# Optimization experiments

Hardware: AMD Instinct MI355X
Metric: run time of the kernel (lower is better)

The kernel has to match this reference:

```python
import jax, jax.numpy as jnp
import numpy as np

OBS, ACT, HID, MIX, TOPK = 64, 16, 256, 16, 4
EPS = 1e-5

def _ln(x, g, b):
    m = jnp.mean(x, axis=-1, keepdims=True)
    v = jnp.mean(jnp.square(x - m), axis=-1, keepdims=True)
    return (x - m) * jax.lax.rsqrt(v + EPS) * g + b

def setup_inputs() -> dict:
    key = jax.random.key(0)
    ks = jax.random.split(key, 12)
    B = 16384
    D = OBS + ACT            # 80
    F = HID * MIX            # 4096
    s = lambda fan_in: 1.0 / np.sqrt(fan_in)
    return {
        "x": jax.random.normal(ks[0], (B, OBS), jnp.float32),
        "a": jax.random.normal(ks[1], (B, ACT), jnp.float32),
        "W1": jax.random.uniform(ks[2], (F, D), jnp.float32, -s(D), s(D)),
        "b1": jnp.zeros((F,), jnp.float32),
        "W2": jax.random.uniform(ks[3], (F, F), jnp.float32, -s(F), s(F)),
        "b2": jnp.zeros((F,), jnp.float32),
        "W3": jax.random.uniform(ks[4], (1, HID), jnp.float32, -s(HID), s(HID)),
        "b3": jnp.zeros((1,), jnp.float32),
        "g1": jnp.ones((F,), jnp.float32),
        "be1": jnp.zeros((F,), jnp.float32),
        "g2": jnp.ones((F,), jnp.float32),
        "be2": jnp.zeros((F,), jnp.float32),
        "Wg": jax.random.uniform(ks[5], (MIX, D), jnp.float32, -s(D), s(D)),
        "bg": jnp.zeros((MIX,), jnp.float32),
    }

def reference(x, a, W1, b1, W2, b2, W3, b3, g1, be1, g2, be2, Wg, bg):
    B = x.shape[0]
    xa = jnp.concatenate([x, a], axis=1)                      # [B, D]
    gate_scores = jax.nn.softmax(xa @ Wg.T + bg, axis=-1)     # [B, MIX]
    topk_vals, topk_idx = jax.lax.top_k(gate_scores, TOPK)    # [B, K]
    # renormalize top-k weights, scatter into dense score tensor
    topk_vals = topk_vals / jnp.sum(topk_vals, axis=-1, keepdims=True)
    scores = jnp.zeros_like(gate_scores).at[
        jnp.arange(B)[:, None], topk_idx].set(topk_vals)      # [B, MIX]
    h = jax.nn.relu(_ln(xa @ W1.T + b1, g1, be1))             # [B, HID*MIX]
    h = jax.nn.relu(_ln(h @ W2.T + b2, g2, be2))              # [B, HID*MIX]
    h = h.reshape(B, HID, MIX)                                # row-major, same as torch
    h = jnp.mean(h * scores[:, None, :], axis=-1)             # [B, HID]
    return h @ W3.T + b3                                      # [B, 1]
```

## Files before the change

### kernel.cpp

```cpp
#include <hip/hip_runtime.h>
#include <stdint.h>

#define OBS 64
#define ACTD 16
#define DIN 80
#define MIX 16
#define FF 4096
#define NB 16384
#define CHUNK 4096
#define KP 96
#define LNEPS 1e-5f

typedef float f32x4 __attribute__((ext_vector_type(4)));
typedef short bf16x8 __attribute__((ext_vector_type(8)));

__device__ __forceinline__ unsigned short f2bf(float f) {
    union { float f; uint32_t u; } v; v.f = f;
    uint32_t u = v.u;
    u += 0x7fff + ((u >> 16) & 1);
    return (unsigned short)(u >> 16);
}
__device__ __forceinline__ float bf2f(unsigned short h) {
    union { uint32_t u; float f; } v; v.u = ((uint32_t)h) << 16;
    return v.f;
}

__global__ __launch_bounds__(256) void k_conv(const float* __restrict__ W,
                                              unsigned short* __restrict__ O, int n4) {
    int i = blockIdx.x * 256 + threadIdx.x;
    if (i >= n4) return;
    float4 v = ((const float4*)W)[i];
    ushort4 o;
    o.x = f2bf(v.x); o.y = f2bf(v.y); o.z = f2bf(v.z); o.w = f2bf(v.w);
    ((ushort4*)O)[i] = o;
}

__global__ __launch_bounds__(256) void k_prep_x(const float* __restrict__ x, const float* __restrict__ a,
                                                unsigned short* __restrict__ xab) {
    int row = blockIdx.x * 256 + threadIdx.x;
    const float4* xp = (const float4*)(x + (size_t)row * OBS);
    unsigned short* o = xab + (size_t)row * KP;
#pragma unroll
    for (int i = 0; i < 16; ++i) {
        float4 v = xp[i];
        ushort4 u; u.x = f2bf(v.x); u.y = f2bf(v.y); u.z = f2bf(v.z); u.w = f2bf(v.w);
        ((ushort4*)o)[i] = u;
    }
    const float4* ap = (const float4*)(a + (size_t)row * ACTD);
#pragma unroll
    for (int i = 0; i < 4; ++i) {
        float4 v = ap[i];
        ushort4 u; u.x = f2bf(v.x); u.y = f2bf(v.y); u.z = f2bf(v.z); u.w = f2bf(v.w);
        ((ushort4*)(o + OBS))[i] = u;
    }
    ushort4 t0; t0.x = 0x3F80; t0.y = 0; t0.z = 0; t0.w = 0;
    ushort4 z;  z.x = 0; z.y = 0; z.z = 0; z.w = 0;
    ((ushort4*)(o + 80))[0] = t0;
    ((ushort4*)(o + 84))[0] = z;
    ((ushort4*)(o + 88))[0] = z;
    ((ushort4*)(o + 92))[0] = z;
}

__global__ __launch_bounds__(256) void k_prep_w1(const float* __restrict__ W1, const float* __restrict__ b1,
                                                 unsigned short* __restrict__ W1b) {
    int f = blockIdx.x * 256 + threadIdx.x;
    const float4* wp = (const float4*)(W1 + (size_t)f * DIN);
    unsigned short* o = W1b + (size_t)f * KP;
#pragma unroll
    for (int i = 0; i < 20; ++i) {
        float4 v = wp[i];
        ushort4 u; u.x = f2bf(v.x); u.y = f2bf(v.y); u.z = f2bf(v.z); u.w = f2bf(v.w);
        ((ushort4*)o)[i] = u;
    }
    ushort4 t0; t0.x = f2bf(b1[f]); t0.y = 0; t0.z = 0; t0.w = 0;
    ushort4 z;  z.x = 0; z.y = 0; z.z = 0; z.w = 0;
    ((ushort4*)(o + 80))[0] = t0;
    ((ushort4*)(o + 84))[0] = z;
    ((ushort4*)(o + 88))[0] = z;
    ((ushort4*)(o + 92))[0] = z;
}

__global__ __launch_bounds__(256) void k_gate(const float* __restrict__ x, const float* __restrict__ a,
                                              const float* __restrict__ Wg, const float* __restrict__ bg,
                                              float* __restrict__ scores) {
    __shared__ float wgs[MIX * DIN];
    __shared__ float bgs[MIX];
    int t = threadIdx.x;
    for (int e = t; e < MIX * DIN; e += 256) wgs[e] = Wg[e];
    if (t < MIX) bgs[t] = bg[t];
    __syncthreads();
    int row = blockIdx.x * 256 + t;
    float xa[DIN];
    const float4* xp = (const float4*)(x + (size_t)row * OBS);
#pragma unroll
    for (int i = 0; i < OBS / 4; ++i) {
        float4 v = xp[i];
        xa[i*4] = v.x; xa[i*4+1] = v.y; xa[i*4+2] = v.z; xa[i*4+3] = v.w;
    }
    const float4* ap = (const float4*)(a + (size_t)row * ACTD);
#pragma unroll
    for (int i = 0; i < ACTD / 4; ++i) {
        float4 v = ap[i];
        xa[OBS+i*4] = v.x; xa[OBS+i*4+1] = v.y; xa[OBS+i*4+2] = v.z; xa[OBS+i*4+3] = v.w;
    }
    double p[MIX];
    double mx = -1e300;
#pragma unroll
    for (int m = 0; m < MIX; ++m) {
        double acc = (double)bgs[m];
#pragma unroll
        for (int k = 0; k < DIN; ++k) acc += (double)xa[k] * (double)wgs[m*DIN + k];
        p[m] = acc;
        if (acc > mx) mx = acc;
    }
#pragma unroll
    for (int m = 0; m < MIX; ++m) p[m] = exp(p[m] - mx);
    unsigned used = 0;
    double s4 = 0.0;
#pragma unroll
    for (int j = 0; j < 4; ++j) {
        int best = 0; double bv = -1.0;
#pragma unroll
        for (int m = 0; m < MIX; ++m)
            if (!((used >> m) & 1) && p[m] > bv) { bv = p[m]; best = m; }
        used |= 1u << best;
        s4 += bv;
    }
    float* so = scores + (size_t)row * MIX;
#pragma unroll
    for (int m = 0; m < MIX; ++m)
        so[m] = ((used >> m) & 1) ? (float)(p[m] / s4) : 0.f;
}

__global__ __launch_bounds__(256) void k_gemm1(const unsigned short* __restrict__ A,
                                               const unsigned short* __restrict__ B,
                                               unsigned short* __restrict__ C,
                                               float* __restrict__ pstats) {
    __shared__ alignas(16) unsigned short As[128 * 32];
    __shared__ alignas(16) unsigned short Bs[128 * 32];
    int t = threadIdx.x;
    int pm = blockIdx.x & 31;
    int pn = blockIdx.x >> 5;
    int lane = t & 63, wid = t >> 6, wm = wid >> 1, wn = wid & 1;

    const unsigned short* Ap = A + (size_t)pm * 128 * KP;
    const unsigned short* Bp = B + (size_t)pn * 128 * KP;

    f32x4 acc[4][4] = {};

    for (int k0 = 0; k0 < KP; k0 += 32) {
#pragma unroll
        for (int i = 0; i < 2; ++i) {
            int u = t + i * 256;
            int row = u >> 2, p = u & 3;
            int ls = p ^ ((row >> 1) & 3);
            __builtin_amdgcn_global_load_lds(
                (const __attribute__((address_space(1))) void*)(Ap + (size_t)row * KP + k0 + ls * 8),
                (__attribute__((address_space(3))) void*)(As + u * 8), 16, 0, 0);
            __builtin_amdgcn_global_load_lds(
                (const __attribute__((address_space(1))) void*)(Bp + (size_t)row * KP + k0 + ls * 8),
                (__attribute__((address_space(3))) void*)(Bs + u * 8), 16, 0, 0);
        }
        __syncthreads();
        bf16x8 af[4], bfr[4];
#pragma unroll
        for (int mf = 0; mf < 4; ++mf) {
            int r = wm * 64 + mf * 16 + (lane & 15);
            int p = (lane >> 4) ^ ((r >> 1) & 3);
            af[mf] = *(const bf16x8*)(As + r * 32 + p * 8);
        }
#pragma unroll
        for (int nf = 0; nf < 4; ++nf) {
            int r = wn * 64 + nf * 16 + (lane & 15);
            int p = (lane >> 4) ^ ((r >> 1) & 3);
            bfr[nf] = *(const bf16x8*)(Bs + r * 32 + p * 8);
        }
#pragma unroll
        for (int mf = 0; mf < 4; ++mf)
#pragma unroll
            for (int nf = 0; nf < 4; ++nf)
                acc[mf][nf] = __builtin_amdgcn_mfma_f32_16x16x32_bf16(af[mf], bfr[nf], acc[mf][nf], 0, 0, 0);
        __syncthreads();
    }

    int rowbase = pm * 128 + wm * 64 + (lane >> 4) * 4;
    int colbase = pn * 128 + wn * 64 + (lane & 15);
#pragma unroll
    for (int mf = 0; mf < 4; ++mf) {
#pragma unroll
        for (int rr = 0; rr < 4; ++rr) {
            float ss = 0.f, qq = 0.f;
#pragma unroll
            for (int nf = 0; nf < 4; ++nf) {
                float v = acc[mf][nf][rr];
                ss += v; qq += v * v;
                C[(size_t)(rowbase + mf * 16 + rr) * FF + colbase + nf * 16] = f2bf(v);
            }
#pragma unroll
            for (int mask = 1; mask <= 8; mask <<= 1) {
                ss += __shfl_xor(ss, mask);
                qq += __shfl_xor(qq, mask);
            }
            if ((lane & 15) == 0) {
                int row = rowbase + mf * 16 + rr;
                int j = pn * 2 + wn;
                pstats[((size_t)row * 64 + j) * 2 + 0] = ss;
                pstats[((size_t)row * 64 + j) * 2 + 1] = qq;
            }
        }
    }
}

__global__ __launch_bounds__(256) void k_ln1(unsigned short* __restrict__ h1,
                                             const float* __restrict__ pstats,
                                             const float* __restrict__ g1, const float* __restrict__ be1) {
    __shared__ float st[8][2];
    int t = threadIdx.x;
    int r0 = blockIdx.x * 8;
    if (t < 8) {
        float s = 0.f, q = 0.f;
        const float* pp = pstats + (size_t)(r0 + t) * 128;
#pragma unroll
        for (int j = 0; j < 64; ++j) { s += pp[j * 2]; q += pp[j * 2 + 1]; }
        float mu = s / (float)FF;
        float var = q / (float)FF - mu * mu;
        st[t][0] = mu;
        st[t][1] = rsqrtf(var + LNEPS);
    }
    __syncthreads();
    int c = t * 16;
    float g[16], b[16];
#pragma unroll
    for (int q = 0; q < 4; ++q) {
        float4 gv = *(const float4*)(g1 + c + q * 4);
        float4 bv = *(const float4*)(be1 + c + q * 4);
        g[q*4] = gv.x; g[q*4+1] = gv.y; g[q*4+2] = gv.z; g[q*4+3] = gv.w;
        b[q*4] = bv.x; b[q*4+1] = bv.y; b[q*4+2] = bv.z; b[q*4+3] = bv.w;
    }
    for (int r = 0; r < 8; ++r) {
        float mu = st[r][0], rs = st[r][1];
        unsigned short* hp = h1 + (size_t)(r0 + r) * FF + c;
        uint4 u0 = *(const uint4*)hp;
        uint4 u1 = *(const uint4*)(hp + 8);
        uint32_t uu[8] = {u0.x, u0.y, u0.z, u0.w, u1.x, u1.y, u1.z, u1.w};
        uint32_t oo[8];
#pragma unroll
        for (int q = 0; q < 8; ++q) {
            float v0 = bf2f((unsigned short)(uu[q] & 0xffff));
            float v1 = bf2f((unsigned short)(uu[q] >> 16));
            float o0 = fmaxf((v0 - mu) * rs * g[q*2]   + b[q*2],   0.f);
            float o1 = fmaxf((v1 - mu) * rs * g[q*2+1] + b[q*2+1], 0.f);
            oo[q] = (uint32_t)f2bf(o0) | ((uint32_t)f2bf(o1) << 16);
        }
        uint4 w0; w0.x = oo[0]; w0.y = oo[1]; w0.z = oo[2]; w0.w = oo[3];
        uint4 w1; w1.x = oo[4]; w1.y = oo[5]; w1.z = oo[6]; w1.w = oo[7];
        *(uint4*)hp = w0;
        *(uint4*)(hp + 8) = w1;
    }
}

__global__ __launch_bounds__(512, 2) void k_gemm2(const unsigned short* __restrict__ A,
                                                  const unsigned short* __restrict__ B,
                                                  unsigned short* __restrict__ C) {
    constexpr int K = FF;
    constexpr int NKT = K / 64;
    __shared__ alignas(16) unsigned short As[2][2][8192];
    __shared__ alignas(16) unsigned short Bs[2][2][8192];

    int t = threadIdx.x;
    int lane = t & 63, wid = t >> 6;
    int wm = wid >> 2, wn = wid & 3;

    int bid = blockIdx.x;
    int xcd = bid & 7, w = bid >> 3;
    int pm = (xcd >> 1) * 4 + (w >> 3);
    int pn = (xcd & 1) * 8 + (w & 7);

    const unsigned short* Ap = A + (size_t)pm * 256 * K;
    const unsigned short* Bp = B + (size_t)pn * 256 * K;

    f32x4 acc[8][4] = {};

#define STAGE_H(bq, kt, H)                                                                 \
    {                                                                                      \
        const unsigned short* gsrc = ((H) < 2) ? Ap : Bp;                                  \
        unsigned short* ldst = ((H) < 2) ? &As[(bq)][(H) & 1][0] : &Bs[(bq)][(H) & 1][0];  \
        _Pragma("unroll")                                                                  \
        for (int i = 0; i < 2; ++i) {                                                      \
            int u = i * 512 + t;                                                           \
            int r = u >> 3, sl = u & 7;                                                    \
            __builtin_amdgcn_global_load_lds(                                              \
                (const __attribute__((address_space(1))) void*)(gsrc +                     \
                    (size_t)(((H) & 1) * 128 + r) * K + (kt) * 64 + ((sl ^ (r & 7)) * 8)), \
                (__attribute__((address_space(3))) void*)(ldst + u * 8), 16, 0, 0);        \
        }                                                                                  \
    }

    STAGE_H(0, 0, 0); STAGE_H(0, 0, 1); STAGE_H(0, 0, 2); STAGE_H(0, 0, 3);
    asm volatile("" ::: "memory");

    for (int kt = 0; kt < NKT; ++kt) {
        int b = kt & 1;
        const unsigned short* Ah = &As[b][wm][0];
        bf16x8 af[4][2], bfr[4][2];

        if (kt < NKT - 1) STAGE_H(b ^ 1, kt + 1, 0);
        if (kt < NKT - 1) asm volatile("s_waitcnt vmcnt(2)" ::: "memory");
        else              asm volatile("s_waitcnt vmcnt(0)" ::: "memory");
        __builtin_amdgcn_s_barrier();
        asm volatile("" ::: "memory");
#pragma unroll
        for (int m = 0; m < 4; ++m) {
            int rr = m * 16 + (lane & 15);
#pragma unroll
            for (int kk = 0; kk < 2; ++kk) {
                int sl = (kk * 4 + (lane >> 4)) ^ (rr & 7);
                af[m][kk] = *(const bf16x8*)(Ah + rr * 64 + sl * 8);
            }
        }
#pragma unroll
        for (int n = 0; n < 4; ++n) {
            int cc = wn * 64 + n * 16 + (lane & 15);
            int hb = cc >> 7, rr = cc & 127;
            const unsigned short* Bh = &Bs[b][hb][0];
#pragma unroll
            for (int kk = 0; kk < 2; ++kk) {
                int sl = (kk * 4 + (lane >> 4)) ^ (rr & 7);
                bfr[n][kk] = *(const bf16x8*)(Bh + rr * 64 + sl * 8);
            }
        }
        __builtin_amdgcn_s_setprio(1);
#pragma unroll
        for (int kk = 0; kk < 2; ++kk)
#pragma unroll
            for (int m = 0; m < 4; ++m)
#pragma unroll
                for (int n = 0; n < 2; ++n)
                    acc[m][n] = __builtin_amdgcn_mfma_f32_16x16x32_bf16(af[m][kk], bfr[n][kk], acc[m][n], 0, 0, 0);
        __builtin_amdgcn_s_setprio(0);
        __builtin_amdgcn_sched_barrier(0);

        if (kt < NKT - 1) STAGE_H(b ^ 1, kt + 1, 1);
        __builtin_amdgcn_s_setprio(1);
#pragma unroll
        for (int kk = 0; kk < 2; ++kk)
#pragma unroll
            for (int m = 0; m < 4; ++m)
#pragma unroll
                for (int n = 2; n < 4; ++n)
                    acc[m][n] = __builtin_amdgcn_mfma_f32_16x16x32_bf16(af[m][kk], bfr[n][kk], acc[m][n], 0, 0, 0);
        __builtin_amdgcn_s_setprio(0);
        __builtin_amdgcn_sched_barrier(0);

        if (kt < NKT - 1) STAGE_H(b ^ 1, kt + 1, 2);
#pragma unroll
        for (int m = 0; m < 4; ++m) {
            int rr = 64 + m * 16 + (lane & 15);
#pragma unroll
            for (int kk = 0; kk < 2; ++kk) {
                int sl = (kk * 4 + (lane >> 4)) ^ (rr & 7);
                af[m][kk] = *(const bf16x8*)(Ah + rr * 64 + sl * 8);
            }
        }
        __builtin_amdgcn_s_setprio(1);
#pragma unroll
        for (int kk = 0; kk < 2; ++kk)
#pragma unroll
            for (int m = 0; m < 4; ++m)
#pragma unroll
                for (int n = 0; n < 2; ++n)
                    acc[4 + m][n] = __builtin_amdgcn_mfma_f32_16x16x32_bf16(af[m][kk], bfr[n][kk], acc[4 + m][n], 0, 0, 0);
        __builtin_amdgcn_s_setprio(0);
        __builtin_amdgcn_sched_barrier(0);

        if (kt < NKT - 1) STAGE_H(b ^ 1, kt + 1, 3);
        __builtin_amdgcn_s_setprio(1);
#pragma unroll
        for (int kk = 0; kk < 2; ++kk)
#pragma unroll
            for (int m = 0; m < 4; ++m)
#pragma unroll
                for (int n = 2; n < 4; ++n)
                    acc[4 + m][n] = __builtin_amdgcn_mfma_f32_16x16x32_bf16(af[m][kk], bfr[n][kk], acc[4 + m][n], 0, 0, 0);
        __builtin_amdgcn_s_setprio(0);
        __builtin_amdgcn_sched_barrier(0);
        asm volatile("" ::: "memory");
        __builtin_amdgcn_s_barrier();
        asm volatile("" ::: "memory");
    }
#undef STAGE_H

    int row0 = pm * 256 + wm * 128 + (lane >> 4) * 4;
    int col0 = pn * 256 + wn * 64 + (lane & 15);
#pragma unroll
    for (int gm = 0; gm < 8; ++gm)
#pragma unroll
        for (int gn = 0; gn < 4; ++gn)
#pragma unroll
            for (int rr = 0; rr < 4; ++rr)
                C[(size_t)(row0 + gm * 16 + rr) * FF + col0 + gn * 16] = f2bf(acc[gm][gn][rr]);
}

__global__ __launch_bounds__(256) void k_epi(const unsigned short* __restrict__ y2,
                                             const float* __restrict__ scores,
                                             const float* __restrict__ b2,
                                             const float* __restrict__ g2, const float* __restrict__ be2,
                                             const float* __restrict__ W3, const float* __restrict__ b3,
                                             float* __restrict__ out) {
    int row = blockIdx.x, t = threadIdx.x;
    int lane = t & 63, wid = t >> 6;
    __shared__ float sS[MIX];
    __shared__ float rA[4], rB[4];
    __shared__ float stats[2];
    const unsigned short* yp = y2 + (size_t)row * FF + t * 16;
    uint4 u0 = *(const uint4*)yp;
    uint4 u1 = *(const uint4*)(yp + 8);
    float v[16];
    v[0]  = bf2f((unsigned short)(u0.x & 0xffff)); v[1]  = bf2f((unsigned short)(u0.x >> 16));
    v[2]  = bf2f((unsigned short)(u0.y & 0xffff)); v[3]  = bf2f((unsigned short)(u0.y >> 16));
    v[4]  = bf2f((unsigned short)(u0.z & 0xffff)); v[5]  = bf2f((unsigned short)(u0.z >> 16));
    v[6]  = bf2f((unsigned short)(u0.w & 0xffff)); v[7]  = bf2f((unsigned short)(u0.w >> 16));
    v[8]  = bf2f((unsigned short)(u1.x & 0xffff)); v[9]  = bf2f((unsigned short)(u1.x >> 16));
    v[10] = bf2f((unsigned short)(u1.y & 0xffff)); v[11] = bf2f((unsigned short)(u1.y >> 16));
    v[12] = bf2f((unsigned short)(u1.z & 0xffff)); v[13] = bf2f((unsigned short)(u1.z >> 16));
    v[14] = bf2f((unsigned short)(u1.w & 0xffff)); v[15] = bf2f((unsigned short)(u1.w >> 16));
    const float* b2p = b2 + t * 16;
#pragma unroll
    for (int blk = 0; blk < 4; ++blk) {
        float4 q = *(const float4*)(b2p + blk * 4);
        v[blk*4+0] += q.x; v[blk*4+1] += q.y; v[blk*4+2] += q.z; v[blk*4+3] += q.w;
    }
    if (t < MIX) sS[t] = scores[(size_t)row * MIX + t];
    float s = 0.f, sq = 0.f;
#pragma unroll
    for (int j = 0; j < 16; ++j) { s += v[j]; sq += v[j] * v[j]; }
#pragma unroll
    for (int off = 32; off >= 1; off >>= 1) {
        s  += __shfl_down(s, off);
        sq += __shfl_down(sq, off);
    }
    if (lane == 0) { rA[wid] = s; rB[wid] = sq; }
    __syncthreads();
    if (t == 0) {
        float S = rA[0] + rA[1] + rA[2] + rA[3];
        float Q = rB[0] + rB[1] + rB[2] + rB[3];
        float mu = S / (float)FF;
        float var = Q / (float)FF - mu * mu;
        stats[0] = mu;
        stats[1] = rsqrtf(var + LNEPS);
    }
    __syncthreads();
    float mu = stats[0], rs = stats[1];
    const float* gp = g2 + t * 16;
    const float* bp = be2 + t * 16;
    float accum = 0.f;
#pragma unroll
    for (int blk = 0; blk < 4; ++blk) {
        float4 gg = *(const float4*)(gp + blk * 4);
        float4 bb = *(const float4*)(bp + blk * 4);
        float ga[4] = {gg.x, gg.y, gg.z, gg.w};
        float ba[4] = {bb.x, bb.y, bb.z, bb.w};
#pragma unroll
        for (int jj = 0; jj < 4; ++jj) {
            int m = blk * 4 + jj;
            float o = (v[m] - mu) * rs * ga[jj] + ba[jj];
            o = fmaxf(o, 0.f);
            accum += o * sS[m];
        }
    }
    float part = accum * W3[t] * 0.0625f;
#pragma unroll
    for (int off = 32; off >= 1; off >>= 1) part += __shfl_down(part, off);
    if (lane == 0) rA[wid] = part;
    __syncthreads();
    if (t == 0) out[row] = rA[0] + rA[1] + rA[2] + rA[3] + b3[0];
}

extern "C" void kernel_launch(void* const* d_in, const int* in_sizes, int n_in,
                              void* d_out, int out_size, void* d_ws, size_t ws_size,
                              hipStream_t stream) {
    const float* x   = (const float*)d_in[0];
    const float* a   = (const float*)d_in[1];
    const float* W1  = (const float*)d_in[2];
    const float* b1  = (const float*)d_in[3];
    const float* W2  = (const float*)d_in[4];
    const float* b2  = (const float*)d_in[5];
    const float* W3  = (const float*)d_in[6];
    const float* b3  = (const float*)d_in[7];
    const float* g1  = (const float*)d_in[8];
    const float* be1 = (const float*)d_in[9];
    const float* g2  = (const float*)d_in[10];
    const float* be2 = (const float*)d_in[11];
    const float* Wg  = (const float*)d_in[12];
    const float* bg  = (const float*)d_in[13];
    float* out = (float*)d_out;

    char* ws = (char*)d_ws;
    unsigned short* W2b    = (unsigned short*)ws;
    float*          scores = (float*)(ws + 33554432ull);
    unsigned short* h1c    = (unsigned short*)(ws + 34603008ull);
    unsigned short* y2c    = (unsigned short*)(ws + 68157440ull);
    unsigned short* xabc   = (unsigned short*)(ws + 68157440ull);
    unsigned short* W1b    = (unsigned short*)(ws + 68157440ull + 786432ull);
    float*          pstats = (float*)(ws + 68157440ull + 1572864ull);

    k_conv<<<(FF * FF / 4 + 255) / 256, 256, 0, stream>>>(W2, W2b, FF * FF / 4);
    k_gate<<<NB / 256, 256, 0, stream>>>(x, a, Wg, bg, scores);

    for (int c = 0; c < NB / CHUNK; ++c) {
        const float* xc = x + (size_t)c * CHUNK * OBS;
        const float* ac = a + (size_t)c * CHUNK * ACTD;
        const float* sc = scores + (size_t)c * CHUNK * MIX;
        float* oc = out + (size_t)c * CHUNK;
        k_prep_x<<<CHUNK / 256, 256, 0, stream>>>(xc, ac, xabc);
        k_prep_w1<<<FF / 256, 256, 0, stream>>>(W1, b1, W1b);
        k_gemm1<<<(CHUNK / 128) * (FF / 128), 256, 0, stream>>>(xabc, W1b, h1c, pstats);
        k_ln1<<<CHUNK / 8, 256, 0, stream>>>(h1c, pstats, g1, be1);
        k_gemm2<<<(CHUNK / 256) * (FF / 256), 512, 0, stream>>>(h1c, W2b, y2c);
        k_epi<<<CHUNK, 256, 0, stream>>>(y2c, sc, b2, g2, be2, W3, b3, oc);
    }
}
```

Baseline: 799.6 us.

## Restructure gemm2 main loop into 8-phase ping-pong pipeline with finer LDS staging

Rewrites the main K loop of the big bf16 GEMM as two unrolled k-tiles per iteration, each split into four barrier-separated phases. Every phase issues one quarter-tile global-to-LDS load and reads only the fragments it needs before its MFMA quarter. Half-tiles of the next-next k-step are prefetched into the buffer just freed, so loads run further ahead of compute. Launch bounds drop from 2 to 1 block per CU, which frees registers at the cost of occupancy. The extra barriers per tile add sync overhead, and the prefetch and buffer-reuse ordering has to be exactly right to stay correct.

Result: slower. 836.1 us (+4.6%).

```diff
diff --git a/kernel.cpp b/kernel.cpp
--- a/kernel.cpp
+++ b/kernel.cpp
@@ -259,7 +259,7 @@
     }
 }
 
-__global__ __launch_bounds__(512, 2) void k_gemm2(const unsigned short* __restrict__ A,
+__global__ __launch_bounds__(512, 1) void k_gemm2(const unsigned short* __restrict__ A,
                                                   const unsigned short* __restrict__ B,
                                                   unsigned short* __restrict__ C) {
     constexpr int K = FF;
@@ -280,6 +280,7 @@
     const unsigned short* Bp = B + (size_t)pn * 256 * K;
 
     f32x4 acc[8][4] = {};
+    bf16x8 af[4][2], bfr[4][2];
 
 #define STAGE_H(bq, kt, H)                                                                 \
     {                                                                                      \
@@ -296,99 +297,86 @@
         }                                                                                  \
     }
 
+#define RD_AF(bq, mh)                                                           \
+    _Pragma("unroll") for (int m = 0; m < 4; ++m) {                             \
+        int rr = (mh) * 64 + m * 16 + (lane & 15);                              \
+        _Pragma("unroll") for (int kk = 0; kk < 2; ++kk) {                      \
+            int sl = (kk * 4 + (lane >> 4)) ^ (rr & 7);                         \
+            af[m][kk] = *(const bf16x8*)(&As[(bq)][wm][0] + rr * 64 + sl * 8);  \
+        }                                                                       \
+    }
+
+#define RD_BF(bq, np)                                                           \
+    _Pragma("unroll") for (int n = 0; n < 2; ++n) {                             \
+        int cc = wn * 64 + ((np) * 2 + n) * 16 + (lane & 15);                   \
+        int hb = cc >> 7, rr = cc & 127;                                        \
+        _Pragma("unroll") for (int kk = 0; kk < 2; ++kk) {                      \
+            int sl = (kk * 4 + (lane >> 4)) ^ (rr & 7);                         \
+            bfr[(np) * 2 + n][kk] = *(const bf16x8*)(&Bs[(bq)][hb][0] + rr * 64 + sl * 8); \
+        }                                                                       \
+    }
+
+#define MFMA_Q(mh, np)                                                          \
+    __builtin_amdgcn_s_barrier();                                               \
+    asm volatile("s_waitcnt lgkmcnt(0)" ::: "memory");                          \
+    __builtin_amdgcn_sched_barrier(0);                                          \
+    __builtin_amdgcn_s_setprio(1);                                              \
+    _Pragma("unroll") for (int kk = 0; kk < 2; ++kk)                            \
+    _Pragma("unroll") for (int m = 0; m < 4; ++m)                               \
+    _Pragma("unroll") for (int n = 0; n < 2; ++n)                               \
+        acc[(mh) * 4 + m][(np) * 2 + n] = __builtin_amdgcn_mfma_f32_16x16x32_bf16( \
+            af[m][kk], bfr[(np) * 2 + n][kk], acc[(mh) * 4 + m][(np) * 2 + n], 0, 0, 0); \
+    __builtin_amdgcn_s_setprio(0);                                              \
+    __builtin_amdgcn_sched_barrier(0);
+
     STAGE_H(0, 0, 0); STAGE_H(0, 0, 1); STAGE_H(0, 0, 2); STAGE_H(0, 0, 3);
-    asm volatile("" ::: "memory");
-
-    for (int kt = 0; kt < NKT; ++kt) {
-        int b = kt & 1;
-        const unsigned short* Ah = &As[b][wm][0];
-        bf16x8 af[4][2], bfr[4][2];
-
-        if (kt < NKT - 1) STAGE_H(b ^ 1, kt + 1, 0);
-        if (kt < NKT - 1) asm volatile("s_waitcnt vmcnt(2)" ::: "memory");
-        else              asm volatile("s_waitcnt vmcnt(0)" ::: "memory");
-        __builtin_amdgcn_s_barrier();
-        asm volatile("" ::: "memory");
-#pragma unroll
-        for (int m = 0; m < 4; ++m) {
-            int rr = m * 16 + (lane & 15);
-#pragma unroll
-            for (int kk = 0; kk < 2; ++kk) {
-                int sl = (kk * 4 + (lane >> 4)) ^ (rr & 7);
-                af[m][kk] = *(const bf16x8*)(Ah + rr * 64 + sl * 8);
-            }
-        }
-#pragma unroll
-        for (int n = 0; n < 4; ++n) {
-            int cc = wn * 64 + n * 16 + (lane & 15);
-            int hb = cc >> 7, rr = cc & 127;
-            const unsigned short* Bh = &Bs[b][hb][0];
-#pragma unroll
-            for (int kk = 0; kk < 2; ++kk) {
-                int sl = (kk * 4 + (lane >> 4)) ^ (rr & 7);
-                bfr[n][kk] = *(const bf16x8*)(Bh + rr * 64 + sl * 8);
-            }
-        }
-        __builtin_amdgcn_s_setprio(1);
-#pragma unroll
-        for (int kk = 0; kk < 2; ++kk)
-#pragma unroll
-            for (int m = 0; m < 4; ++m)
-#pragma unroll
-                for (int n = 0; n < 2; ++n)
-                    acc[m][n] = __builtin_amdgcn_mfma_f32_16x16x32_bf16(af[m][kk], bfr[n][kk], acc[m][n], 0, 0, 0);
-        __builtin_amdgcn_s_setprio(0);
-        __builtin_amdgcn_sched_barrier(0);
-
-        if (kt < NKT - 1) STAGE_H(b ^ 1, kt + 1, 1);
-        __builtin_amdgcn_s_setprio(1);
-#pragma unroll
-        for (int kk = 0; kk < 2; ++kk)
-#pragma unroll
-            for (int m = 0; m < 4; ++m)
-#pragma unroll
-                for (int n = 2; n < 4; ++n)
-                    acc[m][n] = __builtin_amdgcn_mfma_f32_16x16x32_bf16(af[m][kk], bfr[n][kk], acc[m][n], 0, 0, 0);
-        __builtin_amdgcn_s_setprio(0);
-        __builtin_amdgcn_sched_barrier(0);
-
-        if (kt < NKT - 1) STAGE_H(b ^ 1, kt + 1, 2);
-#pragma unroll
-        for (int m = 0; m < 4; ++m) {
-            int rr = 64 + m * 16 + (lane & 15);
-#pragma unroll
-            for (int kk = 0; kk < 2; ++kk) {
-                int sl = (kk * 4 + (lane >> 4)) ^ (rr & 7);
-                af[m][kk] = *(const bf16x8*)(Ah + rr * 64 + sl * 8);
-            }
-        }
-        __builtin_amdgcn_s_setprio(1);
-#pragma unroll
-        for (int kk = 0; kk < 2; ++kk)
-#pragma unroll
-            for (int m = 0; m < 4; ++m)
-#pragma unroll
-                for (int n = 0; n < 2; ++n)
-                    acc[4 + m][n] = __builtin_amdgcn_mfma_f32_16x16x32_bf16(af[m][kk], bfr[n][kk], acc[4 + m][n], 0, 0, 0);
-        __builtin_amdgcn_s_setprio(0);
-        __builtin_amdgcn_sched_barrier(0);
-
-        if (kt < NKT - 1) STAGE_H(b ^ 1, kt + 1, 3);
-        __builtin_amdgcn_s_setprio(1);
-#pragma unroll
-        for (int kk = 0; kk < 2; ++kk)
-#pragma unroll
-            for (int m = 0; m < 4; ++m)
-#pragma unroll
-                for (int n = 2; n < 4; ++n)
-                    acc[4 + m][n] = __builtin_amdgcn_mfma_f32_16x16x32_bf16(af[m][kk], bfr[n][kk], acc[4 + m][n], 0, 0, 0);
-        __builtin_amdgcn_s_setprio(0);
-        __builtin_amdgcn_sched_barrier(0);
-        asm volatile("" ::: "memory");
-        __builtin_amdgcn_s_barrier();
-        asm volatile("" ::: "memory");
+    STAGE_H(1, 1, 2); STAGE_H(1, 1, 3);
+    asm volatile("s_waitcnt vmcnt(4)" ::: "memory");
+    __builtin_amdgcn_s_barrier();
+
+    for (int i = 0; i < NKT / 2; ++i) {
+        int tA = 2 * i + 1;
+        int tB = 2 * i + 2; if (tB > NKT - 1) tB = NKT - 1;
+        int tC = 2 * i + 3; if (tC > NKT - 1) tC = NKT - 1;
+
+        RD_AF(0, 0); RD_BF(0, 0);
+        STAGE_H(1, tA, 0);
+        MFMA_Q(0, 0);
+        __builtin_amdgcn_s_barrier();
+        RD_BF(0, 1);
+        STAGE_H(1, tA, 1);
+        MFMA_Q(0, 1);
+        __builtin_amdgcn_s_barrier();
+        RD_AF(0, 1);
+        STAGE_H(0, tB, 2);
+        MFMA_Q(1, 0);
+        __builtin_amdgcn_s_barrier();
+        STAGE_H(0, tB, 3);
+        MFMA_Q(1, 1);
+        asm volatile("s_waitcnt vmcnt(4)" ::: "memory");
+        __builtin_amdgcn_s_barrier();
+
+        RD_AF(1, 0); RD_BF(1, 0);
+        STAGE_H(0, tB, 0);
+        MFMA_Q(0, 0);
+        __builtin_amdgcn_s_barrier();
+        RD_BF(1, 1);
+        STAGE_H(0, tB, 1);
+        MFMA_Q(0, 1);
+        __builtin_amdgcn_s_barrier();
+        RD_AF(1, 1);
+        STAGE_H(1, tC, 2);
+        MFMA_Q(1, 0);
+        __builtin_amdgcn_s_barrier();
+        STAGE_H(1, tC, 3);
+        MFMA_Q(1, 1);
+        asm volatile("s_waitcnt vmcnt(4)" ::: "memory");
+        __builtin_amdgcn_s_barrier();
     }
 #undef STAGE_H
+#undef RD_AF
+#undef RD_BF
+#undef MFMA_Q
 
     int row0 = pm * 256 + wm * 128 + (lane >> 4) * 4;
     int col0 = pn * 256 + wn * 64 + (lane & 15);
```
